# Performance work log

Measured on AMD Instinct MI355X. Metric: run time of the kernel, lower is better.

## Reference

```python
import jax, jax.numpy as jnp
import numpy as np

B, T, NF, D, H, F, LTXT, V, NL = 256, 24, 12, 256, 8, 512, 128, 30000, 2
LN_EPS = 1e-5

def _make_pe(max_len, d):
    pos = np.arange(max_len)[:, None].astype(np.float32)
    i = np.arange(d)[None, :]
    angle = pos / np.power(10000.0, (2 * (i // 2)).astype(np.float32) / d)
    pe = np.zeros((max_len, d), dtype=np.float32)
    pe[:, 0::2] = np.sin(angle[:, 0::2])
    pe[:, 1::2] = np.cos(angle[:, 1::2])
    return jnp.asarray(pe)

PE = _make_pe(500, D)

def _ln(x, g, b):
    mu = jnp.mean(x, -1, keepdims=True)
    var = jnp.mean((x - mu) ** 2, -1, keepdims=True)
    return (x - mu) / jnp.sqrt(var + LN_EPS) * g + b

def _encoder(x, lengths, in_W, in_b, attn_W, attn_b, ff_W1, ff_b1, ff_W2, ff_b2, ln_g, ln_b):
    # post-LN transformer encoder with length-based padding masks (dropout = eval/identity)
    Bq, S, Dm = x.shape
    dk = Dm // H
    key_mask = jnp.arange(S)[None, :] < lengths[:, None]          # [B,S]
    npad = key_mask[..., None].astype(x.dtype)                    # zero padded positions
    enc = _ln(x @ in_W.T + in_b, ln_g[0], ln_b[0]) + PE[:S]
    for l in range(attn_W.shape[0]):
        q = (enc @ attn_W[l, 0].T + attn_b[l, 0]).reshape(Bq, S, H, dk)
        k = (enc @ attn_W[l, 1].T + attn_b[l, 1]).reshape(Bq, S, H, dk)
        v = (enc @ attn_W[l, 2].T + attn_b[l, 2]).reshape(Bq, S, H, dk)
        scores = jnp.einsum('bqhd,bkhd->bhqk', q, k) / jnp.sqrt(jnp.float32(dk))
        scores = jnp.where(key_mask[:, None, None, :], scores, jnp.float32(-1e9))
        ctx = jnp.einsum('bhqk,bkhd->bqhd', jax.nn.softmax(scores, -1), v).reshape(Bq, S, Dm)
        enc = _ln(ctx @ attn_W[l, 3].T + attn_b[l, 3] + enc, ln_g[1 + 2 * l], ln_b[1 + 2 * l]) * npad
        ff = jax.nn.relu(enc @ ff_W1[l].T + ff_b1[l]) @ ff_W2[l].T + ff_b2[l]
        enc = _ln(ff + enc, ln_g[2 + 2 * l], ln_b[2 + 2 * l]) * npad
    return enc

def _forward(x, h, m, d, x_m, age, gen, dec_w, dec_b, hd_W, hd_b, gru_Wih, gru_Whh, gru_bih, gru_bhh,
             txt_emb, t_in_W, t_in_b, t_attn_W, t_attn_b, t_ff_W1, t_ff_b1, t_ff_W2, t_ff_b2, t_ln_g, t_ln_b,
             f_in_W, f_in_b, f_attn_W, f_attn_b, f_ff_W1, f_ff_b1, f_ff_W2, f_ff_b2, f_ln_g, f_ln_b,
             f_cls, fc1_W, fc1_b, bn_g, bn_b, fc2_W, fc2_b, txts, txt_lengths):
    # GRU-D input decay: 12 independent Linear(1,1) == elementwise affine over feature dim
    x_d = jnp.exp(-jax.nn.relu(d * dec_w + dec_b))                 # [B,T,NF]
    xc = m * x + (1 - m) * x_d * x + (1 - m) * (1 - x_d) * x_m[None, None, :]

    def step(hc, td):
        d_t, x_t, m_t = td                                          # [B,NF] each
        h_d = jnp.exp(-jax.nn.relu(d_t @ hd_W.T + hd_b))            # hidden decay
        hc = h_d * hc
        gi = jnp.concatenate([x_t, m_t], -1) @ gru_Wih.T + gru_bih  # [B,3D]
        gh = hc @ gru_Whh.T + gru_bhh
        ir, iz, inn = jnp.split(gi, 3, -1)
        hr, hz, hn = jnp.split(gh, 3, -1)
        r = jax.nn.sigmoid(ir + hr)
        z = jax.nn.sigmoid(iz + hz)
        n = jnp.tanh(inn + r * hn)
        hc = (1 - z) * n + z * hc
        return hc, hc

    _, emb = jax.lax.scan(step, h, (d.transpose(1, 0, 2), xc.transpose(1, 0, 2), m.transpose(1, 0, 2)))
    emb = emb.transpose(1, 0, 2)                                    # [B,T,D]

    txt_x = txt_emb[txts]                                           # [B,LTXT,D]
    txt_out = _encoder(txt_x, txt_lengths, t_in_W, t_in_b, t_attn_W, t_attn_b,
                       t_ff_W1, t_ff_b1, t_ff_W2, t_ff_b2, t_ln_g, t_ln_b)

    cls_tok = jnp.broadcast_to(f_cls, (emb.shape[0], 1, D))
    seq = jnp.concatenate([cls_tok, emb, txt_out], 1)               # [B,1+T+LTXT,D]
    fin_len = txt_lengths + emb.shape[1] + 1
    fin = _encoder(seq, fin_len, f_in_W, f_in_b, f_attn_W, f_attn_b,
                   f_ff_W1, f_ff_b1, f_ff_W2, f_ff_b2, f_ln_g, f_ln_b)
    cls = fin[:, 0]
    ci = jnp.concatenate([cls, age[:, None], gen[:, None]], 1)      # [B,D+2]
    h1 = jnp.einsum('bd,khd->kbh', ci, fc1_W) + fc1_b[:, None, :]   # 12 task heads
    h1 = (h1 / jnp.sqrt(1.0 + LN_EPS)) * bn_g[:, None, :] + bn_b[:, None, :]  # BatchNorm1d eval (mean 0, var 1)
    h1 = jax.nn.relu(h1)
    out = jnp.einsum('kbh,koh->kbo', h1, fc2_W) + fc2_b[:, None, :]
    return jax.nn.sigmoid(out)                                      # [12,B,1]

def setup_inputs() -> dict:
    key = jax.random.key(0)
    ks = iter(jax.random.split(key, 64))
    def n(shape, s=0.02):
        return jax.random.normal(next(ks), shape, jnp.float32) * s
    inp = {}
    inp['x'] = jax.random.normal(next(ks), (B, T, NF), jnp.float32)
    inp['h'] = jnp.zeros((B, D), jnp.float32)
    inp['m'] = (jax.random.uniform(next(ks), (B, T, NF)) < 0.7).astype(jnp.float32)
    inp['d'] = jax.random.uniform(next(ks), (B, T, NF)) * 5.0
    inp['x_m'] = jax.random.normal(next(ks), (NF,), jnp.float32)
    inp['age'] = jax.random.uniform(next(ks), (B,))
    inp['gen'] = (jax.random.uniform(next(ks), (B,)) < 0.5).astype(jnp.float32)
    inp['input_lengths'] = jnp.full((B,), T, jnp.int32)
    inp['txts'] = jax.random.randint(next(ks), (B, LTXT), 0, V, jnp.int32)
    inp['txt_lengths'] = jax.random.randint(next(ks), (B,), 64, LTXT + 1, jnp.int32)
    inp['dec_w'] = n((NF,), 0.5); inp['dec_b'] = jnp.zeros((NF,), jnp.float32)
    inp['hd_W'] = n((D, NF), 0.1); inp['hd_b'] = jnp.zeros((D,), jnp.float32)
    inp['gru_Wih'] = n((3 * D, 2 * NF), 0.05); inp['gru_Whh'] = n((3 * D, D), 0.05)
    inp['gru_bih'] = jnp.zeros((3 * D,), jnp.float32); inp['gru_bhh'] = jnp.zeros((3 * D,), jnp.float32)
    inp['txt_emb'] = n((V, D), 0.02)
    for p in ('t_', 'f_'):
        inp[p + 'in_W'] = n((D, D)); inp[p + 'in_b'] = jnp.zeros((D,), jnp.float32)
        inp[p + 'attn_W'] = n((NL, 4, D, D)); inp[p + 'attn_b'] = jnp.zeros((NL, 4, D), jnp.float32)
        inp[p + 'ff_W1'] = n((NL, F, D)); inp[p + 'ff_b1'] = jnp.zeros((NL, F), jnp.float32)
        inp[p + 'ff_W2'] = n((NL, D, F)); inp[p + 'ff_b2'] = jnp.zeros((NL, D), jnp.float32)
        inp[p + 'ln_g'] = jnp.ones((1 + 2 * NL, D), jnp.float32)
        inp[p + 'ln_b'] = jnp.zeros((1 + 2 * NL, D), jnp.float32)
    inp['f_cls'] = n((1, 1, D), 1.0)
    inp['fc1_W'] = n((12, 64, D + 2), 0.05); inp['fc1_b'] = jnp.zeros((12, 64), jnp.float32)
    inp['bn_g'] = jnp.ones((12, 64), jnp.float32); inp['bn_b'] = jnp.zeros((12, 64), jnp.float32)
    inp['fc2_W'] = n((12, 1, 64), 0.1); inp['fc2_b'] = jnp.zeros((12, 1), jnp.float32)
    return inp

def reference(x, h, m, d, x_m, age, gen, input_lengths, txts, txt_lengths,
              dec_w, dec_b, hd_W, hd_b, gru_Wih, gru_Whh, gru_bih, gru_bhh, txt_emb,
              t_in_W, t_in_b, t_attn_W, t_attn_b, t_ff_W1, t_ff_b1, t_ff_W2, t_ff_b2, t_ln_g, t_ln_b,
              f_in_W, f_in_b, f_attn_W, f_attn_b, f_ff_W1, f_ff_b1, f_ff_W2, f_ff_b2, f_ln_g, f_ln_b,
              f_cls, fc1_W, fc1_b, bn_g, bn_b, fc2_W, fc2_b):
    return _forward(x, h, m, d, x_m, age, gen, dec_w, dec_b, hd_W, hd_b, gru_Wih, gru_Whh, gru_bih, gru_bhh,
                    txt_emb, t_in_W, t_in_b, t_attn_W, t_attn_b, t_ff_W1, t_ff_b1, t_ff_W2, t_ff_b2, t_ln_g, t_ln_b,
                    f_in_W, f_in_b, f_attn_W, f_attn_b, f_ff_W1, f_ff_b1, f_ff_W2, f_ff_b2, f_ln_g, f_ln_b,
                    f_cls, fc1_W, fc1_b, bn_g, bn_b, fc2_W, fc2_b, txts, txt_lengths)
```

## Files before the change

kernel.cpp:

```cpp
#include <hip/hip_runtime.h>
#include <cstdio>
#include <cstddef>

#define BB    256
#define TT    24
#define NFEAT 12
#define DIM   256
#define NH    8
#define DKH   32
#define FFD   512
#define SEQ_T 128
#define SEQ_F 153
#define NLAY  2

typedef unsigned short u16;
typedef u16   __attribute__((ext_vector_type(8))) u16x8;
typedef short __attribute__((ext_vector_type(8))) s16x8;
typedef float __attribute__((ext_vector_type(4))) f32x4;

__device__ inline u16 f2bf(float f) {
    union { float f; unsigned u; } v; v.f = f;
    unsigned r = v.u + 0x7FFFu + ((v.u >> 16) & 1u);
    return (u16)(r >> 16);
}
__device__ inline float bf2f(u16 h) {
    union { unsigned u; float f; } v; v.u = ((unsigned)h) << 16;
    return v.f;
}

__device__ __forceinline__ void gload16(const u16* g, u16* l) {
    __builtin_amdgcn_global_load_lds(
        (const __attribute__((address_space(1))) unsigned int*)g,
        (__attribute__((address_space(3))) unsigned int*)l, 16, 0, 0);
}

#define PER_ENC_CAST 1114112
__global__ __launch_bounds__(256) void prep_kernel(
    const float* __restrict__ t_in_W, const float* __restrict__ t_attn_W,
    const float* __restrict__ t_ff_W1, const float* __restrict__ t_ff_W2,
    const float* __restrict__ f_in_W, const float* __restrict__ f_attn_W,
    const float* __restrict__ f_ff_W1, const float* __restrict__ f_ff_W2,
    u16* __restrict__ wbf, float* __restrict__ pe,
    const float* __restrict__ Whh, u16* __restrict__ whhT2)
{
    int blk = blockIdx.x;
    if (blk < 8704) {
        int i = blk * 256 + threadIdx.x;
        int e = i >= PER_ENC_CAST;
        int off = i - e * PER_ENC_CAST;
        float v;
        if (off < 65536)       v = (e ? f_in_W   : t_in_W)[off];
        else if (off < 589824) v = (e ? f_attn_W : t_attn_W)[off - 65536];
        else if (off < 851968) v = (e ? f_ff_W1  : t_ff_W1)[off - 589824];
        else                   v = (e ? f_ff_W2  : t_ff_W2)[off - 851968];
        wbf[i] = f2bf(v);
    } else if (blk < 8857) {
        int s = blk - 8704, i = threadIdx.x;
        float e = (float)(2 * (i / 2)) * (1.0f / 256.0f);
        float freq = expf(-e * 9.210340371976184f);
        float ang = (float)s * freq;
        pe[s * 256 + i] = (i & 1) ? cosf(ang) : sinf(ang);
    } else {
        int n = blk - 8857, k = threadIdx.x;
        whhT2[(size_t)(k >> 1) * 1536 + n * 2 + (k & 1)] = f2bf(Whh[(size_t)n * 256 + k]);
    }
}

__global__ __launch_bounds__(768) void grud_kernel(
    const float* __restrict__ x, const float* __restrict__ h0,
    const float* __restrict__ m, const float* __restrict__ dd,
    const float* __restrict__ x_m,
    const float* __restrict__ dec_w, const float* __restrict__ dec_b,
    const float* __restrict__ hd_W, const float* __restrict__ hd_b,
    const float* __restrict__ Wih, const float* __restrict__ bih,
    const u16* __restrict__ WhhT2, const float* __restrict__ bhh,
    float* __restrict__ emb)
{
    int b = blockIdx.x;
    int tid = threadIdx.x;
    int gate = tid >> 8;
    int j = tid & 255;
    __shared__ float hcs[256], hdecs[256], r_s[256], z_s[256];
    __shared__ float dts[12], xcm[24];

    float wih[24];
#pragma unroll
    for (int i = 0; i < 24; i++) wih[i] = Wih[(size_t)tid * 24 + i];
    float bi_ = bih[tid], bh_ = bhh[tid];

    float hdw[12]; float hdb = 0.0f;
    if (tid < 256) {
#pragma unroll
        for (int i = 0; i < 12; i++) hdw[i] = hd_W[tid * 12 + i];
        hdb = hd_b[tid];
        hcs[tid] = h0[(size_t)b * 256 + tid];
    }
    __syncthreads();

    const u16* wcol = WhhT2 + tid * 2;
    for (int t = 0; t < TT; t++) {
        if (tid < 12) {
            size_t idx = ((size_t)b * TT + t) * NFEAT + tid;
            float dv = dd[idx], xv = x[idx], mv = m[idx];
            float xd = expf(-fmaxf(dv * dec_w[tid] + dec_b[tid], 0.0f));
            dts[tid] = dv;
            xcm[tid] = mv * xv + (1.0f - mv) * xd * xv + (1.0f - mv) * (1.0f - xd) * x_m[tid];
            xcm[12 + tid] = mv;
        }
        __syncthreads();
        if (tid < 256) {
            float acc = hdb;
#pragma unroll
            for (int i = 0; i < 12; i++) acc += hdw[i] * dts[i];
            hdecs[tid] = expf(-fmaxf(acc, 0.0f)) * hcs[tid];
        }
        __syncthreads();
        float acc_i = bi_;
#pragma unroll
        for (int i = 0; i < 24; i++) acc_i += wih[i] * xcm[i];
        float a0 = bh_, a1 = 0.0f;
#pragma unroll 8
        for (int k2 = 0; k2 < 128; k2++) {
            unsigned pair = *(const unsigned*)(wcol + (size_t)k2 * 1536);
            a0 = fmaf(bf2f((u16)(pair & 0xFFFFu)), hdecs[2 * k2],     a0);
            a1 = fmaf(bf2f((u16)(pair >> 16)),     hdecs[2 * k2 + 1], a1);
        }
        float acc_h = a0 + a1;
        if (gate == 0) r_s[j] = 1.0f / (1.0f + expf(-(acc_i + acc_h)));
        else if (gate == 1) z_s[j] = 1.0f / (1.0f + expf(-(acc_i + acc_h)));
        __syncthreads();
        if (gate == 2) {
            float n = tanhf(acc_i + r_s[j] * acc_h);
            float hnew = (1.0f - z_s[j]) * n + z_s[j] * hdecs[j];
            hcs[j] = hnew;
            emb[((size_t)b * TT + t) * 256 + j] = hnew;
        }
        __syncthreads();
    }
}

__global__ void gather_kernel(const int* __restrict__ txts, const float* __restrict__ txt_emb,
                              u16* __restrict__ outp) {
    int r = blockIdx.x, i = threadIdx.x;
    outp[(size_t)r * 256 + i] = f2bf(txt_emb[(size_t)txts[r] * 256 + i]);
}

__global__ void build_seq_kernel(const float* __restrict__ emb, const float* __restrict__ encT,
                                 const float* __restrict__ fcls, u16* __restrict__ seq) {
    int r = blockIdx.x, i = threadIdx.x;
    int b = r / SEQ_F, s = r - b * SEQ_F;
    float v;
    if (s == 0)       v = fcls[i];
    else if (s < 25)  v = emb[((size_t)b * TT + (s - 1)) * 256 + i];
    else              v = encT[((size_t)b * SEQ_T + (s - 25)) * 256 + i];
    seq[(size_t)r * 256 + i] = f2bf(v);
}

template <int RELU>
__global__ __launch_bounds__(256) void gemm_bf16_kernel(
    const u16* __restrict__ A, const u16* __restrict__ W,
    const float* __restrict__ bias, u16* __restrict__ Cout,
    int M, int N, int K)
{
    __shared__ u16 As[128 * 32];
    __shared__ u16 Bs[128 * 32];
    const int bm = blockIdx.y * 128, bn = blockIdx.x * 128;
    const int tid = threadIdx.x;
    const int w = tid >> 6, lane = tid & 63;
    const int wm = (w >> 1) * 64, wn = (w & 1) * 64;
    const int l15 = lane & 15, l16 = lane >> 4;
    const int srow = 32 * w + (lane >> 2);
    const int scol = (lane & 3) * 8;
    f32x4 acc[4][4] = {};

    for (int k0 = 0; k0 < K; k0 += 32) {
        __syncthreads();
        const u16* ga = A + (size_t)(bm + srow) * K + k0 + scol;
        const u16* gb = W + (size_t)(bn + srow) * K + k0 + scol;
        gload16(ga,          &As[w * 1024]);
        gload16(ga + 16 * K, &As[w * 1024 + 512]);
        gload16(gb,          &Bs[w * 1024]);
        gload16(gb + 16 * K, &Bs[w * 1024 + 512]);
        __syncthreads();
        s16x8 af[4], bfr[4];
#pragma unroll
        for (int i = 0; i < 4; i++)
            af[i] = *(const s16x8*)&As[(wm + i * 16 + l15) * 32 + l16 * 8];
#pragma unroll
        for (int i = 0; i < 4; i++)
            bfr[i] = *(const s16x8*)&Bs[(wn + i * 16 + l15) * 32 + l16 * 8];
#pragma unroll
        for (int mi = 0; mi < 4; mi++)
#pragma unroll
            for (int ni = 0; ni < 4; ni++)
                acc[mi][ni] = __builtin_amdgcn_mfma_f32_16x16x32_bf16(af[mi], bfr[ni], acc[mi][ni], 0, 0, 0);
    }
#pragma unroll
    for (int mi = 0; mi < 4; mi++)
#pragma unroll
        for (int ni = 0; ni < 4; ni++) {
            int col = bn + wn + ni * 16 + l15;
            float bv = bias[col];
#pragma unroll
            for (int r = 0; r < 4; r++) {
                int row = bm + wm + mi * 16 + l16 * 4 + r;
                float v = acc[mi][ni][r] + bv;
                if (RELU) v = fmaxf(v, 0.0f);
                Cout[(size_t)row * N + col] = f2bf(v);
            }
        }
}

template <int ADDLN>
__global__ __launch_bounds__(512) void gemm_ln_kernel(
    const u16* __restrict__ A, const u16* __restrict__ W,
    const float* __restrict__ bias, const float* __restrict__ res,
    const float* __restrict__ pe,
    const float* __restrict__ g, const float* __restrict__ b2,
    const int* __restrict__ lengths, int len_add, int S,
    float* __restrict__ enc, u16* __restrict__ encbf, int M, int K)
{
    __shared__ u16 As[128 * 32];
    __shared__ u16 Bs[256 * 32];
    __shared__ float2 red[4][128];
    __shared__ float2 red2[128];
    const int bm = blockIdx.x * 128;
    const int tid = threadIdx.x;
    const int w = tid >> 6, lane = tid & 63;
    const int wm = (w >> 2) * 64, wc = w & 3, wn = wc * 64;
    const int l15 = lane & 15, l16 = lane >> 4;
    const int srow = lane >> 2, scol = (lane & 3) * 8;
    f32x4 acc[4][4] = {};

    for (int k0 = 0; k0 < K; k0 += 32) {
        __syncthreads();
        gload16(A + (size_t)(bm + 16 * w + srow) * K + k0 + scol, &As[16 * w * 32]);
        gload16(W + (size_t)(16 * w + srow) * K + k0 + scol,       &Bs[16 * w * 32]);
        gload16(W + (size_t)(128 + 16 * w + srow) * K + k0 + scol, &Bs[(128 + 16 * w) * 32]);
        __syncthreads();
        s16x8 af[4], bfr[4];
#pragma unroll
        for (int i = 0; i < 4; i++)
            af[i] = *(const s16x8*)&As[(wm + i * 16 + l15) * 32 + l16 * 8];
#pragma unroll
        for (int i = 0; i < 4; i++)
            bfr[i] = *(const s16x8*)&Bs[(wn + i * 16 + l15) * 32 + l16 * 8];
#pragma unroll
        for (int mi = 0; mi < 4; mi++)
#pragma unroll
            for (int ni = 0; ni < 4; ni++)
                acc[mi][ni] = __builtin_amdgcn_mfma_f32_16x16x32_bf16(af[mi], bfr[ni], acc[mi][ni], 0, 0, 0);
    }

    float bcol[4];
#pragma unroll
    for (int ni = 0; ni < 4; ni++) bcol[ni] = bias[wn + ni * 16 + l15];
#pragma unroll
    for (int mi = 0; mi < 4; mi++)
#pragma unroll
        for (int ni = 0; ni < 4; ni++)
#pragma unroll
            for (int r = 0; r < 4; r++) {
                float v = acc[mi][ni][r] + bcol[ni];
                if (ADDLN)
                    v += res[(size_t)(bm + wm + mi * 16 + l16 * 4 + r) * 256 + wn + ni * 16 + l15];
                acc[mi][ni][r] = v;
            }
#pragma unroll
    for (int mi = 0; mi < 4; mi++)
#pragma unroll
        for (int r = 0; r < 4; r++) {
            float s = 0.0f, q = 0.0f;
#pragma unroll
            for (int ni = 0; ni < 4; ni++) { float v = acc[mi][ni][r]; s += v; q += v * v; }
#pragma unroll
            for (int off = 1; off <= 8; off <<= 1) {
                s += __shfl_xor(s, off, 64);
                q += __shfl_xor(q, off, 64);
            }
            if (l15 == 0) {
                float2 p; p.x = s; p.y = q;
                red[wc][wm + mi * 16 + l16 * 4 + r] = p;
            }
        }
    __syncthreads();
    if (tid < 128) {
        float s = 0.0f, q = 0.0f;
#pragma unroll
        for (int c = 0; c < 4; c++) { float2 p = red[c][tid]; s += p.x; q += p.y; }
        float mean = s * (1.0f / 256.0f);
        float var = q * (1.0f / 256.0f) - mean * mean;
        float2 o; o.x = mean; o.y = rsqrtf(var + 1e-5f);
        red2[tid] = o;
    }
    __syncthreads();
#pragma unroll
    for (int mi = 0; mi < 4; mi++)
#pragma unroll
        for (int r = 0; r < 4; r++) {
            int lrow = wm + mi * 16 + l16 * 4 + r;
            int grow = bm + lrow;
            float2 mr = red2[lrow];
            int bb = grow / S, sr = grow - bb * S;
            float mask = 1.0f;
            if (ADDLN) mask = (sr < lengths[bb] + len_add) ? 1.0f : 0.0f;
#pragma unroll
            for (int ni = 0; ni < 4; ni++) {
                int col = wn + ni * 16 + l15;
                float o = (acc[mi][ni][r] - mr.x) * mr.y * g[col] + b2[col];
                if (ADDLN) o *= mask;
                else       o += pe[sr * 256 + col];
                enc[(size_t)grow * 256 + col] = o;
                encbf[(size_t)grow * 256 + col] = f2bf(o);
            }
        }
}

__global__ __launch_bounds__(256) void attn_mfma_kernel(
    const u16* __restrict__ qkv, u16* __restrict__ ctx,
    const int* __restrict__ lengths, int len_add, int S)
{
    __shared__ u16 K_lds[160][40];
    __shared__ u16 Vt_lds[32][176];
    __shared__ u16 P_lds[4][16][48];

    const int bh = blockIdx.x;
    const int b = bh >> 3, h = bh & 7;
    const int len = lengths[b] + len_add;
    const int tid = threadIdx.x;
    const int w = tid >> 6;
    const int lane = tid & 63;
    const int l15 = lane & 15, l16 = lane >> 4;

    const u16* kbase = qkv + ((size_t)b * S) * 768 + 256 + h * 32;
    const u16* vbase = kbase + 256;
    for (int chunk = tid; chunk < 160 * 4; chunk += 256) {
        int s = chunk >> 2, d8 = (chunk & 3) * 8;
        u16x8 kv = {}; u16x8 vv = {};
        if (s < S) {
            kv = *(const u16x8*)(kbase + (size_t)s * 768 + d8);
            vv = *(const u16x8*)(vbase + (size_t)s * 768 + d8);
        }
        *(u16x8*)&K_lds[s][d8] = kv;
#pragma unroll
        for (int j = 0; j < 8; j++) Vt_lds[d8 + j][s] = vv[j];
    }
    __syncthreads();

    const f32x4 zero4 = {0.0f, 0.0f, 0.0f, 0.0f};
    const float SCALE = 0.17677669529663687f;

    for (int q0 = w * 16; q0 < S; q0 += 64) {
        const int qr = min(q0 + l15, S - 1);
        s16x8 qf = *(const s16x8*)(qkv + ((size_t)(b * S + qr)) * 768 + h * 32 + l16 * 8);
        f32x4 o0 = zero4, o1 = zero4;
        float mreg = -1e30f, lreg = 0.0f;

        for (int k0 = 0; k0 < len; k0 += 32) {
            s16x8 kf0 = *(const s16x8*)&K_lds[k0 + l15][l16 * 8];
            s16x8 kf1 = *(const s16x8*)&K_lds[k0 + 16 + l15][l16 * 8];
            f32x4 c0 = __builtin_amdgcn_mfma_f32_16x16x32_bf16(kf0, qf, zero4, 0, 0, 0);
            f32x4 c1 = __builtin_amdgcn_mfma_f32_16x16x32_bf16(kf1, qf, zero4, 0, 0, 0);
            float sc[8];
#pragma unroll
            for (int r = 0; r < 4; r++) {
                int key0 = k0 + l16 * 4 + r;
                sc[r]     = (key0 < len)      ? c0[r] * SCALE : -1e30f;
                sc[4 + r] = (key0 + 16 < len) ? c1[r] * SCALE : -1e30f;
            }
            float tmax = sc[0];
#pragma unroll
            for (int i = 1; i < 8; i++) tmax = fmaxf(tmax, sc[i]);
            tmax = fmaxf(tmax, __shfl_xor(tmax, 16, 64));
            tmax = fmaxf(tmax, __shfl_xor(tmax, 32, 64));
            float mnew = fmaxf(mreg, tmax);
            float rescale = expf(mreg - mnew);
            float psum = 0.0f;
            u16 pb[8];
#pragma unroll
            for (int i = 0; i < 8; i++) {
                float p = expf(sc[i] - mnew);
                psum += p;
                pb[i] = f2bf(p);
            }
            psum += __shfl_xor(psum, 16, 64);
            psum += __shfl_xor(psum, 32, 64);
            lreg = lreg * rescale + psum;
            mreg = mnew;
#pragma unroll
            for (int i = 0; i < 4; i++) { o0[i] *= rescale; o1[i] *= rescale; }
#pragma unroll
            for (int r = 0; r < 4; r++) {
                P_lds[w][l15][l16 * 4 + r]      = pb[r];
                P_lds[w][l15][16 + l16 * 4 + r] = pb[4 + r];
            }
            s16x8 pf  = *(const s16x8*)&P_lds[w][l15][l16 * 8];
            s16x8 vf0 = *(const s16x8*)&Vt_lds[l15][k0 + l16 * 8];
            s16x8 vf1 = *(const s16x8*)&Vt_lds[16 + l15][k0 + l16 * 8];
            o0 = __builtin_amdgcn_mfma_f32_16x16x32_bf16(vf0, pf, o0, 0, 0, 0);
            o1 = __builtin_amdgcn_mfma_f32_16x16x32_bf16(vf1, pf, o1, 0, 0, 0);
        }

        float inv = 1.0f / lreg;
        int qg = q0 + l15;
        if (qg < S) {
            size_t ob = ((size_t)(b * S + qg)) * 256 + h * 32;
#pragma unroll
            for (int r = 0; r < 4; r++) {
                ctx[ob + l16 * 4 + r]      = f2bf(o0[r] * inv);
                ctx[ob + 16 + l16 * 4 + r] = f2bf(o1[r] * inv);
            }
        }
    }
}

__global__ __launch_bounds__(64) void classifier_kernel(
    const float* __restrict__ encF, const float* __restrict__ age, const float* __restrict__ gen,
    const float* __restrict__ fc1_W, const float* __restrict__ fc1_b,
    const float* __restrict__ bn_g, const float* __restrict__ bn_b,
    const float* __restrict__ fc2_W, const float* __restrict__ fc2_b,
    float* __restrict__ outp)
{
    int k = blockIdx.x, b = blockIdx.y, t = threadIdx.x;
    const float* cls = encF + (size_t)b * SEQ_F * 256;
    const float* wrow = fc1_W + ((size_t)k * 64 + t) * 258;
    float acc = fc1_b[k * 64 + t];
    for (int d2 = 0; d2 < 256; d2++) acc += cls[d2] * wrow[d2];
    acc += age[b] * wrow[256] + gen[b] * wrow[257];
    const float RSQ = 0.99999500003749980e0f;
    acc = acc * RSQ * bn_g[k * 64 + t] + bn_b[k * 64 + t];
    acc = fmaxf(acc, 0.0f);
    float p = acc * fc2_W[k * 64 + t];
#pragma unroll
    for (int o = 32; o >= 1; o >>= 1) p += __shfl_xor(p, o, 64);
    if (t == 0) outp[k * 256 + b] = 1.0f / (1.0f + expf(-(p + fc2_b[k])));
}

struct WB { const u16 *inW, *attnW, *ff1W, *ff2W; };

static void run_encoder(float* enc, u16* enc_bf,
                        u16* actx_b, u16* scr_b,
                        const WB& wb, const float* pe, int S,
                        const float* in_b, const float* attn_b,
                        const float* ff_b1, const float* ff_b2,
                        const float* ln_g, const float* ln_b,
                        const int* lengths, int len_add, hipStream_t stream)
{
    int M = BB * S;
    int MB = M / 128;
    dim3 g512(512 / 128, MB), g768(768 / 128, MB);
    gemm_ln_kernel<0><<<MB, 512, 0, stream>>>(actx_b, wb.inW, in_b, nullptr, pe,
                                              ln_g, ln_b, lengths, len_add, S,
                                              enc, enc_bf, M, 256);
    for (int l = 0; l < NLAY; l++) {
        const u16* wqkv = wb.attnW + (size_t)l * 4 * 65536;
        const u16* wout = wb.attnW + ((size_t)l * 4 + 3) * 65536;
        const float* bqkv = attn_b + (size_t)l * 4 * 256;
        const float* bout = attn_b + ((size_t)l * 4 + 3) * 256;
        gemm_bf16_kernel<0><<<g768, 256, 0, stream>>>(enc_bf, wqkv, bqkv, scr_b, M, 768, 256);
        attn_mfma_kernel<<<BB * NH, 256, 0, stream>>>(scr_b, actx_b, lengths, len_add, S);
        gemm_ln_kernel<1><<<MB, 512, 0, stream>>>(actx_b, wout, bout, enc, nullptr,
                                                  ln_g + (1 + 2 * l) * 256, ln_b + (1 + 2 * l) * 256,
                                                  lengths, len_add, S, enc, enc_bf, M, 256);
        gemm_bf16_kernel<1><<<g512, 256, 0, stream>>>(enc_bf, wb.ff1W + (size_t)l * 512 * 256,
                                                      ff_b1 + l * 512, scr_b, M, 512, 256);
        gemm_ln_kernel<1><<<MB, 512, 0, stream>>>(scr_b, wb.ff2W + (size_t)l * 256 * 512,
                                                  ff_b2 + l * 256, enc, nullptr,
                                                  ln_g + (2 + 2 * l) * 256, ln_b + (2 + 2 * l) * 256,
                                                  lengths, len_add, S, enc, enc_bf, M, 512);
    }
}

extern "C" void kernel_launch(void* const* d_in, const int* in_sizes, int n_in,
                              void* d_out, int out_size, void* d_ws, size_t ws_size,
                              hipStream_t stream)
{
    const float* x        = (const float*)d_in[0];
    const float* h0       = (const float*)d_in[1];
    const float* m        = (const float*)d_in[2];
    const float* dd       = (const float*)d_in[3];
    const float* x_m      = (const float*)d_in[4];
    const float* age      = (const float*)d_in[5];
    const float* gen      = (const float*)d_in[6];
    const int*   txts     = (const int*)d_in[8];
    const int*   txt_len  = (const int*)d_in[9];
    const float* dec_w    = (const float*)d_in[10];
    const float* dec_b    = (const float*)d_in[11];
    const float* hd_W     = (const float*)d_in[12];
    const float* hd_b     = (const float*)d_in[13];
    const float* gru_Wih  = (const float*)d_in[14];
    const float* gru_Whh  = (const float*)d_in[15];
    const float* gru_bih  = (const float*)d_in[16];
    const float* gru_bhh  = (const float*)d_in[17];
    const float* txt_emb  = (const float*)d_in[18];
    const float* t_in_W   = (const float*)d_in[19];
    const float* t_in_b   = (const float*)d_in[20];
    const float* t_attn_W = (const float*)d_in[21];
    const float* t_attn_b = (const float*)d_in[22];
    const float* t_ff_W1  = (const float*)d_in[23];
    const float* t_ff_b1  = (const float*)d_in[24];
    const float* t_ff_W2  = (const float*)d_in[25];
    const float* t_ff_b2  = (const float*)d_in[26];
    const float* t_ln_g   = (const float*)d_in[27];
    const float* t_ln_b   = (const float*)d_in[28];
    const float* f_in_W   = (const float*)d_in[29];
    const float* f_in_b   = (const float*)d_in[30];
    const float* f_attn_W = (const float*)d_in[31];
    const float* f_attn_b = (const float*)d_in[32];
    const float* f_ff_W1  = (const float*)d_in[33];
    const float* f_ff_b1  = (const float*)d_in[34];
    const float* f_ff_W2  = (const float*)d_in[35];
    const float* f_ff_b2  = (const float*)d_in[36];
    const float* f_ln_g   = (const float*)d_in[37];
    const float* f_ln_b   = (const float*)d_in[38];
    const float* f_cls    = (const float*)d_in[39];
    const float* fc1_W    = (const float*)d_in[40];
    const float* fc1_b    = (const float*)d_in[41];
    const float* bn_g     = (const float*)d_in[42];
    const float* bn_b     = (const float*)d_in[43];
    const float* fc2_W    = (const float*)d_in[44];
    const float* fc2_b    = (const float*)d_in[45];
    float* outp = (float*)d_out;

    const size_t O_PE    = 0;
    const size_t O_WHHT  = 40960;
    const size_t O_EMB   = 237568;
    const size_t O_ENCT  = 1810432;
    const size_t O_ENCF  = 10199040;
    const size_t O_SCR   = 20226048;
    const size_t O_ACTX  = 35266560;
    const size_t O_ENCBF = 45293568;
    const size_t O_WBF   = 50307072;
    const size_t TOTALF  = 51421184;

    if (ws_size < TOTALF * sizeof(float)) {
        fprintf(stderr, "kernel_launch: ws_size %zu < required %zu bytes\n",
                ws_size, TOTALF * sizeof(float));
        return;
    }
    float* ws    = (float*)d_ws;
    float* pe    = ws + O_PE;
    u16*   whhT2 = (u16*)(ws + O_WHHT);
    float* emb   = ws + O_EMB;
    float* encT  = ws + O_ENCT;
    float* encF  = ws + O_ENCF;
    u16*   scr_b = (u16*)(ws + O_SCR);
    u16*   actx_b= (u16*)(ws + O_ACTX);
    u16*   encbf = (u16*)(ws + O_ENCBF);
    u16*   wbf   = (u16*)(ws + O_WBF);

    const size_t PER_ENC = PER_ENC_CAST;
    WB wbT = { wbf + 0,       wbf + 65536,           wbf + 589824,           wbf + 851968 };
    WB wbF = { wbf + PER_ENC, wbf + PER_ENC + 65536, wbf + PER_ENC + 589824, wbf + PER_ENC + 851968 };

    prep_kernel<<<9625, 256, 0, stream>>>(t_in_W, t_attn_W, t_ff_W1, t_ff_W2,
                                          f_in_W, f_attn_W, f_ff_W1, f_ff_W2,
                                          wbf, pe, gru_Whh, whhT2);

    grud_kernel<<<BB, 768, 0, stream>>>(x, h0, m, dd, x_m, dec_w, dec_b, hd_W, hd_b,
                                        gru_Wih, gru_bih, whhT2, gru_bhh, emb);

    gather_kernel<<<BB * SEQ_T, 256, 0, stream>>>(txts, txt_emb, actx_b);
    run_encoder(encT, encbf, actx_b, scr_b, wbT, pe, SEQ_T,
                t_in_b, t_attn_b, t_ff_b1, t_ff_b2, t_ln_g, t_ln_b, txt_len, 0, stream);

    build_seq_kernel<<<BB * SEQ_F, 256, 0, stream>>>(emb, encT, f_cls, actx_b);
    run_encoder(encF, encbf, actx_b, scr_b, wbF, pe, SEQ_F,
                f_in_b, f_attn_b, f_ff_b1, f_ff_b2, f_ln_g, f_ln_b, txt_len, 25, stream);

    classifier_kernel<<<dim3(12, BB), 64, 0, stream>>>(encF, age, gen, fc1_W, fc1_b,
                                                       bn_g, bn_b, fc2_W, fc2_b, outp);
}
```

Baseline: 945.7 us.

## Double-buffer GEMM LDS tiles and vectorize GRU recurrent and weight-cast loads

Both bf16 GEMM kernels now keep two LDS buffers and issue the global-to-LDS loads for the next K tile before running the MFMAs on the current one. This hides load latency and drops one barrier per iteration, at the cost of doubling LDS use, which may lower occupancy. The GRU recurrent weights are repacked four per column group so each thread does one 8-byte weight load and one float4 hidden-state load per step, with four accumulators. The prep cast kernel also converts four floats per thread.

Result: slower. 981.7 us (+3.8%).

```diff
diff --git a/kernel.cpp b/kernel.cpp
--- a/kernel.cpp
+++ b/kernel.cpp
@@ -41,28 +41,31 @@
     const float* __restrict__ f_in_W, const float* __restrict__ f_attn_W,
     const float* __restrict__ f_ff_W1, const float* __restrict__ f_ff_W2,
     u16* __restrict__ wbf, float* __restrict__ pe,
-    const float* __restrict__ Whh, u16* __restrict__ whhT2)
+    const float* __restrict__ Whh, u16* __restrict__ whhT4)
 {
     int blk = blockIdx.x;
-    if (blk < 8704) {
-        int i = blk * 256 + threadIdx.x;
+    if (blk < 2176) {
+        int i = (blk * 256 + threadIdx.x) * 4;
         int e = i >= PER_ENC_CAST;
         int off = i - e * PER_ENC_CAST;
-        float v;
-        if (off < 65536)       v = (e ? f_in_W   : t_in_W)[off];
-        else if (off < 589824) v = (e ? f_attn_W : t_attn_W)[off - 65536];
-        else if (off < 851968) v = (e ? f_ff_W1  : t_ff_W1)[off - 589824];
-        else                   v = (e ? f_ff_W2  : t_ff_W2)[off - 851968];
-        wbf[i] = f2bf(v);
-    } else if (blk < 8857) {
-        int s = blk - 8704, i = threadIdx.x;
+        const float* src;
+        if (off < 65536)       { src = (e ? f_in_W   : t_in_W)   + off; }
+        else if (off < 589824) { src = (e ? f_attn_W : t_attn_W) + off - 65536; }
+        else if (off < 851968) { src = (e ? f_ff_W1  : t_ff_W1)  + off - 589824; }
+        else                   { src = (e ? f_ff_W2  : t_ff_W2)  + off - 851968; }
+        float4 v = *(const float4*)src;
+        ushort4 o;
+        o.x = f2bf(v.x); o.y = f2bf(v.y); o.z = f2bf(v.z); o.w = f2bf(v.w);
+        *(ushort4*)&wbf[i] = o;
+    } else if (blk < 2329) {
+        int s = blk - 2176, i = threadIdx.x;
         float e = (float)(2 * (i / 2)) * (1.0f / 256.0f);
         float freq = expf(-e * 9.210340371976184f);
         float ang = (float)s * freq;
         pe[s * 256 + i] = (i & 1) ? cosf(ang) : sinf(ang);
     } else {
-        int n = blk - 8857, k = threadIdx.x;
-        whhT2[(size_t)(k >> 1) * 1536 + n * 2 + (k & 1)] = f2bf(Whh[(size_t)n * 256 + k]);
+        int n = blk - 2329, k = threadIdx.x;
+        whhT4[(size_t)(k >> 2) * 3072 + n * 4 + (k & 3)] = f2bf(Whh[(size_t)n * 256 + k]);
     }
 }
 
@@ -73,14 +76,16 @@
     const float* __restrict__ dec_w, const float* __restrict__ dec_b,
     const float* __restrict__ hd_W, const float* __restrict__ hd_b,
     const float* __restrict__ Wih, const float* __restrict__ bih,
-    const u16* __restrict__ WhhT2, const float* __restrict__ bhh,
+    const u16* __restrict__ WhhT4, const float* __restrict__ bhh,
     float* __restrict__ emb)
 {
     int b = blockIdx.x;
     int tid = threadIdx.x;
     int gate = tid >> 8;
     int j = tid & 255;
-    __shared__ float hcs[256], hdecs[256], r_s[256], z_s[256];
+    __shared__ float hcs[256];
+    __shared__ __align__(16) float hdecs[256];
+    __shared__ float r_s[256], z_s[256];
     __shared__ float dts[12], xcm[24];
 
     float wih[24];
@@ -97,7 +102,7 @@
     }
     __syncthreads();
 
-    const u16* wcol = WhhT2 + tid * 2;
+    const u16* wcol4 = WhhT4 + tid * 4;
     for (int t = 0; t < TT; t++) {
         if (tid < 12) {
             size_t idx = ((size_t)b * TT + t) * NFEAT + tid;
@@ -118,14 +123,20 @@
         float acc_i = bi_;
 #pragma unroll
         for (int i = 0; i < 24; i++) acc_i += wih[i] * xcm[i];
-        float a0 = bh_, a1 = 0.0f;
+        float a0 = bh_, a1 = 0.0f, a2 = 0.0f, a3 = 0.0f;
 #pragma unroll 8
-        for (int k2 = 0; k2 < 128; k2++) {
-            unsigned pair = *(const unsigned*)(wcol + (size_t)k2 * 1536);
-            a0 = fmaf(bf2f((u16)(pair & 0xFFFFu)), hdecs[2 * k2],     a0);
-            a1 = fmaf(bf2f((u16)(pair >> 16)),     hdecs[2 * k2 + 1], a1);
-        }
-        float acc_h = a0 + a1;
+        for (int k4 = 0; k4 < 64; k4++) {
+            uint2 wp = *(const uint2*)(wcol4 + (size_t)k4 * 3072);
+            float4 hv = *(const float4*)&hdecs[4 * k4];
+            union { unsigned u; float f; } c0, c1, c2, c3;
+            c0.u = wp.x << 16; c1.u = wp.x & 0xFFFF0000u;
+            c2.u = wp.y << 16; c3.u = wp.y & 0xFFFF0000u;
+            a0 = fmaf(c0.f, hv.x, a0);
+            a1 = fmaf(c1.f, hv.y, a1);
+            a2 = fmaf(c2.f, hv.z, a2);
+            a3 = fmaf(c3.f, hv.w, a3);
+        }
+        float acc_h = (a0 + a1) + (a2 + a3);
         if (gate == 0) r_s[j] = 1.0f / (1.0f + expf(-(acc_i + acc_h)));
         else if (gate == 1) z_s[j] = 1.0f / (1.0f + expf(-(acc_i + acc_h)));
         __syncthreads();
@@ -162,8 +173,8 @@
     const float* __restrict__ bias, u16* __restrict__ Cout,
     int M, int N, int K)
 {
-    __shared__ u16 As[128 * 32];
-    __shared__ u16 Bs[128 * 32];
+    __shared__ u16 As[2][128 * 32];
+    __shared__ u16 Bs[2][128 * 32];
     const int bm = blockIdx.y * 128, bn = blockIdx.x * 128;
     const int tid = threadIdx.x;
     const int w = tid >> 6, lane = tid & 63;
@@ -173,28 +184,38 @@
     const int scol = (lane & 3) * 8;
     f32x4 acc[4][4] = {};
 
+    const u16* ga0 = A + (size_t)(bm + srow) * K + scol;
+    const u16* gb0 = W + (size_t)(bn + srow) * K + scol;
+
+#define STAGE_G(buf, kk)                                        \
+    do {                                                        \
+        gload16(ga0 + (kk),          &As[buf][w * 1024]);       \
+        gload16(ga0 + (kk) + 16 * K, &As[buf][w * 1024 + 512]); \
+        gload16(gb0 + (kk),          &Bs[buf][w * 1024]);       \
+        gload16(gb0 + (kk) + 16 * K, &Bs[buf][w * 1024 + 512]); \
+    } while (0)
+
+    STAGE_G(0, 0);
+    __syncthreads();
+    int cur = 0;
     for (int k0 = 0; k0 < K; k0 += 32) {
-        __syncthreads();
-        const u16* ga = A + (size_t)(bm + srow) * K + k0 + scol;
-        const u16* gb = W + (size_t)(bn + srow) * K + k0 + scol;
-        gload16(ga,          &As[w * 1024]);
-        gload16(ga + 16 * K, &As[w * 1024 + 512]);
-        gload16(gb,          &Bs[w * 1024]);
-        gload16(gb + 16 * K, &Bs[w * 1024 + 512]);
-        __syncthreads();
+        if (k0 + 32 < K) STAGE_G(cur ^ 1, k0 + 32);
         s16x8 af[4], bfr[4];
 #pragma unroll
         for (int i = 0; i < 4; i++)
-            af[i] = *(const s16x8*)&As[(wm + i * 16 + l15) * 32 + l16 * 8];
+            af[i] = *(const s16x8*)&As[cur][(wm + i * 16 + l15) * 32 + l16 * 8];
 #pragma unroll
         for (int i = 0; i < 4; i++)
-            bfr[i] = *(const s16x8*)&Bs[(wn + i * 16 + l15) * 32 + l16 * 8];
+            bfr[i] = *(const s16x8*)&Bs[cur][(wn + i * 16 + l15) * 32 + l16 * 8];
 #pragma unroll
         for (int mi = 0; mi < 4; mi++)
 #pragma unroll
             for (int ni = 0; ni < 4; ni++)
                 acc[mi][ni] = __builtin_amdgcn_mfma_f32_16x16x32_bf16(af[mi], bfr[ni], acc[mi][ni], 0, 0, 0);
-    }
+        __syncthreads();
+        cur ^= 1;
+    }
+#undef STAGE_G
 #pragma unroll
     for (int mi = 0; mi < 4; mi++)
 #pragma unroll
@@ -220,8 +241,8 @@
     const int* __restrict__ lengths, int len_add, int S,
     float* __restrict__ enc, u16* __restrict__ encbf, int M, int K)
 {
-    __shared__ u16 As[128 * 32];
-    __shared__ u16 Bs[256 * 32];
+    __shared__ u16 As[2][128 * 32];
+    __shared__ u16 Bs[2][256 * 32];
     __shared__ float2 red[4][128];
     __shared__ float2 red2[128];
     const int bm = blockIdx.x * 128;
@@ -232,25 +253,38 @@
     const int srow = lane >> 2, scol = (lane & 3) * 8;
     f32x4 acc[4][4] = {};
 
+    const u16* ga0 = A + (size_t)(bm + 16 * w + srow) * K + scol;
+    const u16* gb0 = W + (size_t)(16 * w + srow) * K + scol;
+    const u16* gb1 = W + (size_t)(128 + 16 * w + srow) * K + scol;
+
+#define STAGE_L(buf, kk)                                      \
+    do {                                                      \
+        gload16(ga0 + (kk), &As[buf][16 * w * 32]);           \
+        gload16(gb0 + (kk), &Bs[buf][16 * w * 32]);           \
+        gload16(gb1 + (kk), &Bs[buf][(128 + 16 * w) * 32]);   \
+    } while (0)
+
+    STAGE_L(0, 0);
+    __syncthreads();
+    int cur = 0;
     for (int k0 = 0; k0 < K; k0 += 32) {
-        __syncthreads();
-        gload16(A + (size_t)(bm + 16 * w + srow) * K + k0 + scol, &As[16 * w * 32]);
-        gload16(W + (size_t)(16 * w + srow) * K + k0 + scol,       &Bs[16 * w * 32]);
-        gload16(W + (size_t)(128 + 16 * w + srow) * K + k0 + scol, &Bs[(128 + 16 * w) * 32]);
-        __syncthreads();
+        if (k0 + 32 < K) STAGE_L(cur ^ 1, k0 + 32);
         s16x8 af[4], bfr[4];
 #pragma unroll
         for (int i = 0; i < 4; i++)
-            af[i] = *(const s16x8*)&As[(wm + i * 16 + l15) * 32 + l16 * 8];
+            af[i] = *(const s16x8*)&As[cur][(wm + i * 16 + l15) * 32 + l16 * 8];
 #pragma unroll
         for (int i = 0; i < 4; i++)
-            bfr[i] = *(const s16x8*)&Bs[(wn + i * 16 + l15) * 32 + l16 * 8];
+            bfr[i] = *(const s16x8*)&Bs[cur][(wn + i * 16 + l15) * 32 + l16 * 8];
 #pragma unroll
         for (int mi = 0; mi < 4; mi++)
 #pragma unroll
             for (int ni = 0; ni < 4; ni++)
                 acc[mi][ni] = __builtin_amdgcn_mfma_f32_16x16x32_bf16(af[mi], bfr[ni], acc[mi][ni], 0, 0, 0);
-    }
+        __syncthreads();
+        cur ^= 1;
+    }
+#undef STAGE_L
 
     float bcol[4];
 #pragma unroll
@@ -540,7 +574,7 @@
     }
     float* ws    = (float*)d_ws;
     float* pe    = ws + O_PE;
-    u16*   whhT2 = (u16*)(ws + O_WHHT);
+    u16*   whhT4 = (u16*)(ws + O_WHHT);
     float* emb   = ws + O_EMB;
     float* encT  = ws + O_ENCT;
     float* encF  = ws + O_ENCF;
@@ -553,12 +587,12 @@
     WB wbT = { wbf + 0,       wbf + 65536,           wbf + 589824,           wbf + 851968 };
     WB wbF = { wbf + PER_ENC, wbf + PER_ENC + 65536, wbf + PER_ENC + 589824, wbf + PER_ENC + 851968 };
 
-    prep_kernel<<<9625, 256, 0, stream>>>(t_in_W, t_attn_W, t_ff_W1, t_ff_W2,
+    prep_kernel<<<3097, 256, 0, stream>>>(t_in_W, t_attn_W, t_ff_W1, t_ff_W2,
                                           f_in_W, f_attn_W, f_ff_W1, f_ff_W2,
-                                          wbf, pe, gru_Whh, whhT2);
+                                          wbf, pe, gru_Whh, whhT4);
 
     grud_kernel<<<BB, 768, 0, stream>>>(x, h0, m, dd, x_m, dec_w, dec_b, hd_W, hd_b,
-                                        gru_Wih, gru_bih, whhT2, gru_bhh, emb);
+                                        gru_Wih, gru_bih, whhT4, gru_bhh, emb);
 
     gather_kernel<<<BB * SEQ_T, 256, 0, stream>>>(txts, txt_emb, actx_b);
     run_encoder(encT, encbf, actx_b, scr_b, wbT, pe, SEQ_T,
```
